# Optimization experiments

Hardware: AMD Instinct MI355X
Metric: run time of the kernel (lower is better)

Reference implementation:

```python
import jax, jax.numpy as jnp
import numpy as np

D_MODEL = 768
NUM_HEADS = 12
D_HEAD = D_MODEL // NUM_HEADS


def setup_inputs() -> dict:
    key = jax.random.key(0)
    ks = jax.random.split(key, 11)
    B, S = 1, 4096
    s = 1.0 / np.sqrt(D_MODEL)
    inp = {
        'q': jax.random.normal(ks[0], (B, S, D_MODEL), dtype=jnp.float32),
        'k': jax.random.normal(ks[1], (B, S, D_MODEL), dtype=jnp.float32),
        'v': jax.random.normal(ks[2], (B, S, D_MODEL), dtype=jnp.float32),
        'wq': jax.random.normal(ks[3], (D_MODEL, D_MODEL), dtype=jnp.float32) * s,
        'bq': jnp.zeros((D_MODEL,), dtype=jnp.float32),
        'wk': jax.random.normal(ks[4], (D_MODEL, D_MODEL), dtype=jnp.float32) * s,
        'bk': jnp.zeros((D_MODEL,), dtype=jnp.float32),
        'wv': jax.random.normal(ks[5], (D_MODEL, D_MODEL), dtype=jnp.float32) * s,
        'bv': jnp.zeros((D_MODEL,), dtype=jnp.float32),
        'wo': jax.random.normal(ks[6], (D_MODEL, D_MODEL), dtype=jnp.float32) * s,
        'bo': jnp.zeros((D_MODEL,), dtype=jnp.float32),
    }
    return inp


def reference(q, k, v, wq, bq, wk, bk, wv, bv, wo, bo):
    B, S, _ = q.shape
    # linear projections (torch Linear: x @ W^T + b)
    qh = (q @ wq.T + bq).reshape(B, S, NUM_HEADS, D_HEAD).transpose(0, 2, 1, 3)
    kh = (k @ wk.T + bk).reshape(B, S, NUM_HEADS, D_HEAD).transpose(0, 2, 1, 3)
    vh = (v @ wv.T + bv).reshape(B, S, NUM_HEADS, D_HEAD).transpose(0, 2, 1, 3)
    scores = jnp.einsum('bhqd,bhkd->bhqk', qh, kh) / jnp.sqrt(jnp.float32(D_HEAD))
    causal = jnp.tril(jnp.ones((S, S), dtype=bool))  # [S,S] causal mask
    scores = jnp.where(causal, scores, jnp.finfo(scores.dtype).min)
    attn = jax.nn.softmax(scores, axis=-1)  # dropout omitted (eval mode)
    out = jnp.einsum('bhqk,bhkd->bhqd', attn, vh)
    out = out.transpose(0, 2, 1, 3).reshape(B, S, D_MODEL)
    return out @ wo.T + bo
```

## Files before the change

### kernel.cpp

```cpp
#include <hip/hip_runtime.h>
#include <stdint.h>

typedef __attribute__((ext_vector_type(8))) short short8;
typedef __attribute__((ext_vector_type(4))) float float4v;
typedef __attribute__((ext_vector_type(2))) uint32_t uint32x2;
typedef __attribute__((ext_vector_type(4))) uint32_t uint32x4;

__device__ __forceinline__ unsigned short f2bf(float f) {
  union { float f; uint32_t u; } v;
  v.f = f;
  uint32_t u = v.u;
  return (unsigned short)((u + 0x7fffu + ((u >> 16) & 1u)) >> 16);
}

__device__ __forceinline__ uint32_t pkbf(float a, float b) {
#if __has_builtin(__builtin_amdgcn_cvt_pk_bf16_f32)
  typedef __attribute__((ext_vector_type(2))) __bf16 bf16x2;
  bf16x2 r = __builtin_amdgcn_cvt_pk_bf16_f32(a, b);
  union { bf16x2 v; uint32_t u; } c;
  c.v = r;
  return c.u;
#else
  return (uint32_t)f2bf(a) | ((uint32_t)f2bf(b) << 16);
#endif
}

__device__ __forceinline__ float fexp2(float x) {
#if __has_builtin(__builtin_amdgcn_exp2f)
  return __builtin_amdgcn_exp2f(x);
#else
  return exp2f(x);
#endif
}

__device__ __forceinline__ void gll16(const unsigned short* g, unsigned short* l) {
  __builtin_amdgcn_global_load_lds(
      (const __attribute__((address_space(1))) void*)g,
      (__attribute__((address_space(3))) void*)l, 16, 0, 0);
}

struct CvtArgs {
  const float* src[7];
  unsigned short* dst[7];
};

__global__ __launch_bounds__(256) void cvt_all(CvtArgs a) {
  const int bid = blockIdx.x;
  int t, off;
  if (bid < 4608) { t = bid / 1536; off = bid - t * 1536; }
  else { const int b2 = bid - 4608; t = 3 + b2 / 288; off = b2 - (t - 3) * 288; }
  const size_t i = (size_t)off * 256 + threadIdx.x;
  const float4v* p = (const float4v*)(a.src[t] + i * 8);
  float4v x = p[0], y = p[1];
  uint32x4 o;
  o[0] = pkbf(x[0], x[1]);
  o[1] = pkbf(x[2], x[3]);
  o[2] = pkbf(y[0], y[1]);
  o[3] = pkbf(y[2], y[3]);
  *(uint32x4*)(a.dst[t] + i * 8) = o;
}

__global__ __launch_bounds__(256) void gemm_qkv(
    const unsigned short* __restrict__ xq, const unsigned short* __restrict__ xk,
    const unsigned short* __restrict__ xv,
    const unsigned short* __restrict__ wqb, const unsigned short* __restrict__ wkb,
    const unsigned short* __restrict__ wvb,
    const float* __restrict__ bq, const float* __restrict__ bk,
    const float* __restrict__ bv,
    unsigned short* __restrict__ Qp, unsigned short* __restrict__ Kp,
    unsigned short* __restrict__ Vt, float qscale)
{
  __shared__ unsigned short As[128 * 64];
  __shared__ unsigned short Ws[128 * 64];
  const int z = blockIdx.z;
  const unsigned short* A = z == 0 ? xq : z == 1 ? xk : xv;
  const unsigned short* W = z == 0 ? wqb : z == 1 ? wkb : wvb;
  const float* bias = z == 0 ? bq : z == 1 ? bk : bv;
  const int M = 4096, N = 768, K = 768;
  const int tid = threadIdx.x, wave = tid >> 6, lane = tid & 63;
  const int g = lane >> 4, l16 = lane & 15;
  const int sw = l16 & 7;
  const int m0 = blockIdx.x * 128, n0 = blockIdx.y * 128;
  const int wn = (wave >> 1) * 64, wm = (wave & 1) * 64;
  const int srow0 = wave * 32 + (lane >> 3);
  const int skg = lane & 7;

  float4v acc[4][4] = {};

  for (int k0 = 0; k0 < K; k0 += 64) {
    if (k0) __syncthreads();
    #pragma unroll
    for (int c = 0; c < 4; ++c) {
      const int row = srow0 + c * 8;
      const int kg = skg ^ (row & 7);
      gll16(A + (size_t)(m0 + row) * K + k0 + kg * 8, &As[(wave * 32 + c * 8) * 64]);
      gll16(W + (size_t)(n0 + row) * K + k0 + kg * 8, &Ws[(wave * 32 + c * 8) * 64]);
    }
    __syncthreads();
    #pragma unroll
    for (int kk = 0; kk < 2; ++kk) {
      const int kg = ((kk * 4 + g) ^ sw) * 8;
      short8 xf[4], wf[4];
      #pragma unroll
      for (int t = 0; t < 4; ++t) {
        xf[t] = *(const short8*)&As[(wm + t * 16 + l16) * 64 + kg];
        wf[t] = *(const short8*)&Ws[(wn + t * 16 + l16) * 64 + kg];
      }
      if (z < 2) {
        #pragma unroll
        for (int i = 0; i < 4; ++i)
          #pragma unroll
          for (int j = 0; j < 4; ++j)
            acc[i][j] = __builtin_amdgcn_mfma_f32_16x16x32_bf16(wf[i], xf[j], acc[i][j], 0, 0, 0);
      } else {
        #pragma unroll
        for (int i = 0; i < 4; ++i)
          #pragma unroll
          for (int j = 0; j < 4; ++j)
            acc[i][j] = __builtin_amdgcn_mfma_f32_16x16x32_bf16(xf[i], wf[j], acc[i][j], 0, 0, 0);
      }
    }
  }

  if (z < 2) {
    unsigned short* O = z == 0 ? Qp : Kp;
    const float osc = z == 0 ? qscale : 1.0f;
    #pragma unroll
    for (int i = 0; i < 4; ++i) {
      const int nb = n0 + wn + i * 16 + 4 * g;
      const float4v bb = *(const float4v*)&bias[nb];
      #pragma unroll
      for (int j = 0; j < 4; ++j) {
        const int m = m0 + wm + j * 16 + l16;
        uint32x2 pk;
        pk[0] = pkbf((acc[i][j][0] + bb[0]) * osc, (acc[i][j][1] + bb[1]) * osc);
        pk[1] = pkbf((acc[i][j][2] + bb[2]) * osc, (acc[i][j][3] + bb[3]) * osc);
        *(uint32x2*)(O + (size_t)m * N + nb) = pk;
      }
    }
  } else {
    #pragma unroll
    for (int j = 0; j < 4; ++j) {
      const int n = n0 + wn + j * 16 + l16;
      const float bb = bias[n];
      #pragma unroll
      for (int i = 0; i < 4; ++i) {
        const int mb = m0 + wm + i * 16 + 4 * g;
        uint32x2 pk;
        pk[0] = pkbf(acc[i][j][0] + bb, acc[i][j][1] + bb);
        pk[1] = pkbf(acc[i][j][2] + bb, acc[i][j][3] + bb);
        *(uint32x2*)(Vt + (size_t)n * M + mb) = pk;
      }
    }
  }
}

__global__ __launch_bounds__(256, 3) void flash_part(
    const unsigned short* __restrict__ Qp,
    const unsigned short* __restrict__ Kp,
    const unsigned short* __restrict__ Vt,
    unsigned short* __restrict__ Opart,
    float* __restrict__ lpart)
{
  __shared__ unsigned short lds_k[2][64 * 64];
  __shared__ unsigned short lds_v[2][64 * 64];
  __shared__ unsigned short lds_p[4][32 * 64];
  const int S = 4096, DM = 768;

  const int gid = blockIdx.x;
  const int h = gid % 12;
  const int e = 79 - gid / 12;
  int t, c;
  if (e < 8)       { t = e;                c = 0; }
  else if (e < 24) { t = 8 + (e - 8) / 2;  c = (e - 8) % 2; }
  else if (e < 48) { t = 16 + (e - 24) / 3; c = (e - 24) % 3; }
  else             { t = 24 + (e - 48) / 4; c = (e - 48) % 4; }
  const int kb0 = c * 16;
  const int kbe = min(kb0 + 16, 2 * t + 2);

  const int tid = threadIdx.x, wave = tid >> 6, lane = tid & 63;
  const int g = lane >> 4, l16 = lane & 15;
  const int sw = l16 & 7;
  const int qbase = t * 128 + wave * 32;

  short8 qf[2][2];
  #pragma unroll
  for (int qc = 0; qc < 2; ++qc) {
    const unsigned short* qp = Qp + (size_t)(qbase + qc * 16 + l16) * DM + h * 64;
    qf[qc][0] = *(const short8*)(qp + g * 8);
    qf[qc][1] = *(const short8*)(qp + 32 + g * 8);
  }

  float4v o[2][4] = {};
  float lsum[2] = {0.0f, 0.0f};

  const int strow = wave * 16 + (lane >> 3);
  const int skg = lane & 7;

  #pragma unroll
  for (int cc = 0; cc < 2; ++cc) {
    const int row = strow + cc * 8;
    const int kg = skg ^ (row & 7);
    gll16(Kp + (size_t)(kb0 * 64 + row) * DM + h * 64 + kg * 8,
          &lds_k[0][(wave * 16 + cc * 8) * 64]);
    gll16(Vt + (size_t)(h * 64 + row) * S + kb0 * 64 + kg * 8,
          &lds_v[0][(wave * 16 + cc * 8) * 64]);
  }
  __syncthreads();

  for (int kb = kb0; kb < kbe; ++kb) {
    const int cur = kb & 1;
    if (kb + 1 < kbe) {
      const int nb = cur ^ 1;
      #pragma unroll
      for (int cc = 0; cc < 2; ++cc) {
        const int row = strow + cc * 8;
        const int kg = skg ^ (row & 7);
        gll16(Kp + (size_t)((kb + 1) * 64 + row) * DM + h * 64 + kg * 8,
              &lds_k[nb][(wave * 16 + cc * 8) * 64]);
        gll16(Vt + (size_t)(h * 64 + row) * S + (kb + 1) * 64 + kg * 8,
              &lds_v[nb][(wave * 16 + cc * 8) * 64]);
      }
    }
    const unsigned short* kc = lds_k[cur];
    const unsigned short* vc = lds_v[cur];

    float4v sf[2][4];
    #pragma unroll
    for (int mt = 0; mt < 4; ++mt) {
      short8 ka0 = *(const short8*)&kc[(mt * 16 + l16) * 64 + ((0 + g) ^ sw) * 8];
      short8 ka1 = *(const short8*)&kc[(mt * 16 + l16) * 64 + ((4 + g) ^ sw) * 8];
      #pragma unroll
      for (int qc = 0; qc < 2; ++qc) {
        float4v a = {};
        a = __builtin_amdgcn_mfma_f32_16x16x32_bf16(ka0, qf[qc][0], a, 0, 0, 0);
        a = __builtin_amdgcn_mfma_f32_16x16x32_bf16(ka1, qf[qc][1], a, 0, 0, 0);
        sf[qc][mt] = a;
      }
    }

    if ((kb + 1) * 64 > qbase) {
      #pragma unroll
      for (int qc = 0; qc < 2; ++qc) {
        const int q = qbase + qc * 16 + l16;
        #pragma unroll
        for (int mt = 0; mt < 4; ++mt)
          #pragma unroll
          for (int rr = 0; rr < 4; ++rr) {
            const int key = kb * 64 + mt * 16 + 4 * g + rr;
            sf[qc][mt][rr] = (key <= q) ? sf[qc][mt][rr] : -1e30f;
          }
      }
    }

    #pragma unroll
    for (int qc = 0; qc < 2; ++qc)
      #pragma unroll
      for (int mt = 0; mt < 4; ++mt)
        #pragma unroll
        for (int rr = 0; rr < 4; ++rr) {
          const float pe = fexp2(sf[qc][mt][rr]);
          sf[qc][mt][rr] = pe;
          lsum[qc] += pe;
        }

    unsigned short* pw = lds_p[wave];
    #pragma unroll
    for (int qc = 0; qc < 2; ++qc) {
      #pragma unroll
      for (int mt = 0; mt < 4; ++mt) {
        uint32x2 pp;
        pp[0] = pkbf(sf[qc][mt][0], sf[qc][mt][1]);
        pp[1] = pkbf(sf[qc][mt][2], sf[qc][mt][3]);
        const int kgp = mt * 2 + (g >> 1);
        *(uint32x2*)&pw[(qc * 16 + l16) * 64 + ((kgp ^ sw) * 8) + (g & 1) * 4] = pp;
      }
    }
    __builtin_amdgcn_wave_barrier();

    #pragma unroll
    for (int ks2 = 0; ks2 < 2; ++ks2) {
      short8 pf[2];
      #pragma unroll
      for (int qc = 0; qc < 2; ++qc)
        pf[qc] = *(const short8*)&pw[(qc * 16 + l16) * 64 + (((ks2 * 4 + g) ^ sw) * 8)];
      #pragma unroll
      for (int dt = 0; dt < 4; ++dt) {
        short8 va = *(const short8*)&vc[(dt * 16 + l16) * 64 + (((ks2 * 4 + g) ^ sw) * 8)];
        #pragma unroll
        for (int qc = 0; qc < 2; ++qc)
          o[qc][dt] = __builtin_amdgcn_mfma_f32_16x16x32_bf16(va, pf[qc], o[qc][dt], 0, 0, 0);
      }
    }

    __syncthreads();
  }

  const int slot = (h * 32 + t) * 4 + c;
  unsigned short* ob = Opart + (size_t)slot * 8192;
  #pragma unroll
  for (int qc = 0; qc < 2; ++qc) {
    float L = lsum[qc];
    L += __shfl_xor(L, 16);
    L += __shfl_xor(L, 32);
    const int ql = wave * 32 + qc * 16 + l16;
    if (g == 0) lpart[slot * 128 + ql] = L;
    #pragma unroll
    for (int dt = 0; dt < 4; ++dt) {
      uint32x2 ov;
      ov[0] = pkbf(o[qc][dt][0], o[qc][dt][1]);
      ov[1] = pkbf(o[qc][dt][2], o[qc][dt][3]);
      *(uint32x2*)(ob + (size_t)ql * 64 + dt * 16 + 4 * g) = ov;
    }
  }
}

__global__ __launch_bounds__(256) void flash_combine(
    const unsigned short* __restrict__ Opart, const float* __restrict__ lpart,
    unsigned short* __restrict__ AO)
{
  const int t = blockIdx.x, h = blockIdx.y;
  const int nc = (2 * t + 17) >> 4;
  const int slot0 = (h * 32 + t) * 4;
  const int tid = threadIdx.x;
  const int qr = tid >> 2, dc = (tid & 3) * 16;
  #pragma unroll
  for (int it = 0; it < 2; ++it) {
    const int ql = it * 64 + qr;
    float acc[16];
    #pragma unroll
    for (int j = 0; j < 16; ++j) acc[j] = 0.0f;
    float lsum = 0.0f;
    for (int cc = 0; cc < nc; ++cc) {
      const int slot = slot0 + cc;
      lsum += lpart[slot * 128 + ql];
      const uint32x4* p = (const uint32x4*)(Opart + (size_t)slot * 8192 + ql * 64 + dc);
      uint32x4 w0 = p[0], w1 = p[1];
      #pragma unroll
      for (int j = 0; j < 4; ++j) {
        union { uint32_t u; float f; } lo, hi;
        lo.u = w0[j] << 16; hi.u = w0[j] & 0xffff0000u;
        acc[2 * j] += lo.f; acc[2 * j + 1] += hi.f;
        lo.u = w1[j] << 16; hi.u = w1[j] & 0xffff0000u;
        acc[8 + 2 * j] += lo.f; acc[8 + 2 * j + 1] += hi.f;
      }
    }
    const float inv = 1.0f / lsum;
    uint32x4 o0, o1;
    #pragma unroll
    for (int j = 0; j < 4; ++j) {
      o0[j] = pkbf(acc[2 * j] * inv, acc[2 * j + 1] * inv);
      o1[j] = pkbf(acc[8 + 2 * j] * inv, acc[8 + 2 * j + 1] * inv);
    }
    unsigned short* dst = AO + (size_t)(t * 128 + ql) * 768 + h * 64 + dc;
    *(uint32x4*)dst = o0;
    *(uint32x4*)(dst + 8) = o1;
  }
}

__global__ __launch_bounds__(256) void gemm_out(
    const unsigned short* __restrict__ A, const unsigned short* __restrict__ W,
    const float* __restrict__ bias, float* __restrict__ Out)
{
  __shared__ unsigned short As[128 * 64];
  __shared__ unsigned short Ws[128 * 64];
  const int N = 768, K = 768;
  const int tid = threadIdx.x, wave = tid >> 6, lane = tid & 63;
  const int g = lane >> 4, l16 = lane & 15;
  const int sw = l16 & 7;
  const int m0 = blockIdx.x * 128, n0 = blockIdx.y * 128;
  const int wn = (wave >> 1) * 64, wm = (wave & 1) * 64;
  const int srow0 = wave * 32 + (lane >> 3);
  const int skg = lane & 7;

  float4v acc[4][4] = {};

  for (int k0 = 0; k0 < K; k0 += 64) {
    if (k0) __syncthreads();
    #pragma unroll
    for (int c = 0; c < 4; ++c) {
      const int row = srow0 + c * 8;
      const int kg = skg ^ (row & 7);
      gll16(A + (size_t)(m0 + row) * K + k0 + kg * 8, &As[(wave * 32 + c * 8) * 64]);
      gll16(W + (size_t)(n0 + row) * K + k0 + kg * 8, &Ws[(wave * 32 + c * 8) * 64]);
    }
    __syncthreads();
    #pragma unroll
    for (int kk = 0; kk < 2; ++kk) {
      const int kg = ((kk * 4 + g) ^ sw) * 8;
      short8 xf[4], wf[4];
      #pragma unroll
      for (int t = 0; t < 4; ++t) {
        xf[t] = *(const short8*)&As[(wm + t * 16 + l16) * 64 + kg];
        wf[t] = *(const short8*)&Ws[(wn + t * 16 + l16) * 64 + kg];
      }
      #pragma unroll
      for (int i = 0; i < 4; ++i)
        #pragma unroll
        for (int j = 0; j < 4; ++j)
          acc[i][j] = __builtin_amdgcn_mfma_f32_16x16x32_bf16(wf[i], xf[j], acc[i][j], 0, 0, 0);
    }
  }

  #pragma unroll
  for (int i = 0; i < 4; ++i) {
    const int nb = n0 + wn + i * 16 + 4 * g;
    const float4v bb = *(const float4v*)&bias[nb];
    #pragma unroll
    for (int j = 0; j < 4; ++j) {
      const int m = m0 + wm + j * 16 + l16;
      float4v ov;
      #pragma unroll
      for (int rr = 0; rr < 4; ++rr) ov[rr] = acc[i][j][rr] + bb[rr];
      *(float4v*)(Out + (size_t)m * N + nb) = ov;
    }
  }
}

extern "C" void kernel_launch(void* const* d_in, const int* in_sizes, int n_in,
                              void* d_out, int out_size, void* d_ws, size_t ws_size,
                              hipStream_t stream) {
  const float* q  = (const float*)d_in[0];
  const float* k  = (const float*)d_in[1];
  const float* v  = (const float*)d_in[2];
  const float* wq = (const float*)d_in[3];
  const float* bq = (const float*)d_in[4];
  const float* wk = (const float*)d_in[5];
  const float* bk = (const float*)d_in[6];
  const float* wv = (const float*)d_in[7];
  const float* bv = (const float*)d_in[8];
  const float* wo = (const float*)d_in[9];
  const float* bo = (const float*)d_in[10];
  float* out = (float*)d_out;

  const int S = 4096, D = 768;
  unsigned short* Qp    = (unsigned short*)d_ws;
  unsigned short* Kp    = Qp  + (size_t)S * D;
  unsigned short* Vt    = Kp  + (size_t)S * D;
  unsigned short* AO    = Vt  + (size_t)S * D;
  unsigned short* xq    = AO  + (size_t)S * D;
  unsigned short* xk    = xq  + (size_t)S * D;
  unsigned short* xv    = xk  + (size_t)S * D;
  unsigned short* wqb   = xv  + (size_t)S * D;
  unsigned short* wkb   = wqb + (size_t)D * D;
  unsigned short* wvb   = wkb + (size_t)D * D;
  unsigned short* wob   = wvb + (size_t)D * D;
  unsigned short* Opart = wob + (size_t)D * D;
  float*          lpart = (float*)(Opart + (size_t)1536 * 8192);

  CvtArgs ca;
  ca.src[0] = q;  ca.dst[0] = xq;
  ca.src[1] = k;  ca.dst[1] = xk;
  ca.src[2] = v;  ca.dst[2] = xv;
  ca.src[3] = wq; ca.dst[3] = wqb;
  ca.src[4] = wk; ca.dst[4] = wkb;
  ca.src[5] = wv; ca.dst[5] = wvb;
  ca.src[6] = wo; ca.dst[6] = wob;

  const float SC = 0.125f * 1.44269504089f;
  dim3 blk(256);
  cvt_all<<<dim3(5760), blk, 0, stream>>>(ca);
  gemm_qkv<<<dim3(32, 6, 3), blk, 0, stream>>>(xq, xk, xv, wqb, wkb, wvb,
                                               bq, bk, bv, Qp, Kp, Vt, SC);
  flash_part<<<dim3(960), blk, 0, stream>>>(Qp, Kp, Vt, Opart, lpart);
  flash_combine<<<dim3(32, 12), blk, 0, stream>>>(Opart, lpart, AO);
  gemm_out<<<dim3(32, 6), blk, 0, stream>>>(AO, wob, bo, out);
}
```

Before: 213.2 us.

## Keep softmax probabilities in registers and use 16x16x16 MFMA for PV

Removes the per-wave LDS staging buffer for the bf16 probability tile. The PV product now uses 16x16x16 bf16 MFMAs whose B operand layout matches the QK^T accumulator layout, so P feeds straight from registers. This drops the LDS writes, the wave barrier and the LDS reads. It also frees LDS and raises the occupancy hint from 3 to 4 blocks per SM. The trade is twice as many smaller MFMA instructions and 8-byte V loads instead of 16-byte ones, plus register pressure under the tighter launch bound.

```diff
diff --git a/kernel.cpp b/kernel.cpp
--- a/kernel.cpp
+++ b/kernel.cpp
@@ -2,6 +2,7 @@
 #include <stdint.h>
 
 typedef __attribute__((ext_vector_type(8))) short short8;
+typedef __attribute__((ext_vector_type(4))) short short4v;
 typedef __attribute__((ext_vector_type(4))) float float4v;
 typedef __attribute__((ext_vector_type(2))) uint32_t uint32x2;
 typedef __attribute__((ext_vector_type(4))) uint32_t uint32x4;
@@ -30,6 +31,17 @@
   return __builtin_amdgcn_exp2f(x);
 #else
   return exp2f(x);
+#endif
+}
+
+__device__ __forceinline__ float4v mfma16bf(short4v a, short4v b, float4v c) {
+#if __has_builtin(__builtin_amdgcn_mfma_f32_16x16x16bf16_1k)
+  return __builtin_amdgcn_mfma_f32_16x16x16bf16_1k(a, b, c, 0, 0, 0);
+#else
+  float4v d;
+  asm("v_mfma_f32_16x16x16_bf16 %0, %1, %2, %3"
+      : "=v"(d) : "v"(a), "v"(b), "v"(c));
+  return d;
 #endif
 }
 
@@ -155,7 +167,7 @@
   }
 }
 
-__global__ __launch_bounds__(256, 3) void flash_part(
+__global__ __launch_bounds__(256, 4) void flash_part(
     const unsigned short* __restrict__ Qp,
     const unsigned short* __restrict__ Kp,
     const unsigned short* __restrict__ Vt,
@@ -164,7 +176,6 @@
 {
   __shared__ unsigned short lds_k[2][64 * 64];
   __shared__ unsigned short lds_v[2][64 * 64];
-  __shared__ unsigned short lds_p[4][32 * 64];
   const int S = 4096, DM = 768;
 
   const int gid = blockIdx.x;
@@ -253,43 +264,31 @@
       }
     }
 
+    short4v pb[2][4];
     #pragma unroll
     for (int qc = 0; qc < 2; ++qc)
       #pragma unroll
-      for (int mt = 0; mt < 4; ++mt)
+      for (int mt = 0; mt < 4; ++mt) {
+        float4v pe;
         #pragma unroll
         for (int rr = 0; rr < 4; ++rr) {
-          const float pe = fexp2(sf[qc][mt][rr]);
-          sf[qc][mt][rr] = pe;
-          lsum[qc] += pe;
+          pe[rr] = fexp2(sf[qc][mt][rr]);
+          lsum[qc] += pe[rr];
         }
-
-    unsigned short* pw = lds_p[wave];
-    #pragma unroll
-    for (int qc = 0; qc < 2; ++qc) {
-      #pragma unroll
-      for (int mt = 0; mt < 4; ++mt) {
-        uint32x2 pp;
-        pp[0] = pkbf(sf[qc][mt][0], sf[qc][mt][1]);
-        pp[1] = pkbf(sf[qc][mt][2], sf[qc][mt][3]);
-        const int kgp = mt * 2 + (g >> 1);
-        *(uint32x2*)&pw[(qc * 16 + l16) * 64 + ((kgp ^ sw) * 8) + (g & 1) * 4] = pp;
-      }
-    }
-    __builtin_amdgcn_wave_barrier();
-
-    #pragma unroll
-    for (int ks2 = 0; ks2 < 2; ++ks2) {
-      short8 pf[2];
-      #pragma unroll
-      for (int qc = 0; qc < 2; ++qc)
-        pf[qc] = *(const short8*)&pw[(qc * 16 + l16) * 64 + (((ks2 * 4 + g) ^ sw) * 8)];
+        union { uint32x2 u; short4v s; } cv;
+        cv.u[0] = pkbf(pe[0], pe[1]);
+        cv.u[1] = pkbf(pe[2], pe[3]);
+        pb[qc][mt] = cv.s;
+      }
+
+    #pragma unroll
+    for (int ms = 0; ms < 4; ++ms) {
+      const int slot = ((2 * ms + (g >> 1)) ^ sw) * 8 + (g & 1) * 4;
       #pragma unroll
       for (int dt = 0; dt < 4; ++dt) {
-        short8 va = *(const short8*)&vc[(dt * 16 + l16) * 64 + (((ks2 * 4 + g) ^ sw) * 8)];
-        #pragma unroll
-        for (int qc = 0; qc < 2; ++qc)
-          o[qc][dt] = __builtin_amdgcn_mfma_f32_16x16x32_bf16(va, pf[qc], o[qc][dt], 0, 0, 0);
+        short4v va = *(const short4v*)&vc[(dt * 16 + l16) * 64 + slot];
+        o[0][dt] = mfma16bf(va, pb[0][ms], o[0][dt]);
+        o[1][dt] = mfma16bf(va, pb[1][ms], o[1][dt]);
       }
     }
 
```

New measurement: 211.6 us. No clear change (-0.7%).
